# Kernel tuning notes

Hardware: AMD Instinct MI355X
Metric: run time of the kernel (lower is better)

## Reference

```python
import jax, jax.numpy as jnp
import numpy as np

V, D, DC, L, K, H, ND, S, B = 16, 256, 128, 3, 16, 4, 3, 900, 16
HD = D // H
DMETA = 17           # [confidence(1) | layer_id(8) | iter(4) | pass(4)]
DSLOT = DC + DMETA
MAX_ITERS, MAX_PASSES, WRITE_TOK = 2, 2, 64
FLOATS = ['token_embed','segment_embed','slot_embeddings','layer_id_embeddings',
          'Wq_read','Wk_read','Wv_read','Wg_read','bg_read','Wqkv','Wo',
          'Wwk','Wwv','Wwg','bwg','Wout','bout','prev_answer_embed','Wfb','bfb']


def setup_inputs():
    key = jax.random.key(0)
    ks = jax.random.split(key, 24)
    n = lambda i, shape: 0.02 * jax.random.normal(ks[i], shape, dtype=jnp.float32)
    return dict(
        demo_inputs=jax.random.randint(ks[0], (B, ND, S), 0, V),
        demo_outputs=jax.random.randint(ks[1], (B, ND, S), 0, V),
        test_input=jax.random.randint(ks[2], (B, S), 0, V),
        token_embed=n(3, (V, D)), segment_embed=n(4, (2, D)),
        slot_embeddings=n(5, (L, K, DC)), layer_id_embeddings=n(6, (L, 8)),
        Wq_read=n(7, (L, D, DC)), Wk_read=n(8, (L, DSLOT, DC)), Wv_read=n(9, (L, DSLOT, D)),
        Wg_read=n(10, (L, D, 1)), bg_read=jnp.zeros((L, 1)),
        Wqkv=n(11, (L, D, 3 * D)), Wo=n(12, (L, D, D)),
        Wwk=n(13, (L, D, DC)), Wwv=n(14, (L, D, DC)),
        Wwg=n(15, (L, 2 * DC, 1)), bwg=jnp.zeros((L, 1)),
        Wout=n(16, (D, V)), bout=jnp.zeros((V,)),
        prev_answer_embed=n(17, (V, D)),
        Wfb=n(18, (2 * D, D)), bfb=jnp.zeros((D,)),
    )


def make_rope(n, hd):
    inv = 1.0 / (10000.0 ** (jnp.arange(0, hd, 2, dtype=jnp.float32) / hd))
    f = jnp.arange(n, dtype=jnp.float32)[:, None] * inv[None, :]  # [N, hd/2]
    return jnp.cos(f), jnp.sin(f)


def apply_rope(x, cos, sin):  # x: [B,H,N,hd]
    x1, x2 = x[..., ::2], x[..., 1::2]
    r1 = x1 * cos - x2 * sin
    r2 = x1 * sin + x2 * cos
    return jnp.stack([r1, r2], axis=-1).reshape(x.shape)


def layer_step(h, cache, l, it, pas, cos, sin, p):
    Bsz, N, _ = h.shape
    s0 = l * K
    # --- read: cross-attention from sequence to full structured cache ---
    q = h @ p['Wq_read'][l]                                   # [B,N,DC]
    k = cache @ p['Wk_read'][l]                               # [B,LK,DC]
    v = cache @ p['Wv_read'][l]                               # [B,LK,D]
    attn = jax.nn.softmax(jnp.einsum('bnd,bmd->bnm', q, k) / np.float32(np.sqrt(DC)), axis=-1)
    read = jnp.einsum('bnm,bmd->bnd', attn, v)
    rgate = jax.nn.sigmoid(h @ p['Wg_read'][l] + p['bg_read'][l])
    h = h + rgate * read
    # --- linear self-attention with RoPE (use_linear_attention=True) ---
    qh, kh, vh = jnp.split(h @ p['Wqkv'][l], 3, axis=-1)
    heads = lambda x: x.reshape(Bsz, N, H, HD).transpose(0, 2, 1, 3)
    qh, kh, vh = heads(qh), heads(kh), heads(vh)
    qf = jax.nn.elu(apply_rope(qh, cos, sin)) + 1.0
    kf = jax.nn.elu(apply_rope(kh, cos, sin)) + 1.0
    kv = jnp.einsum('bhnd,bhne->bhde', kf, vh)                # [B,H,HD,HD]
    z = 1.0 / (jnp.einsum('bhnd,bhd->bhn', qf, kf.sum(axis=2)) + 1e-6)
    att = jnp.einsum('bhnd,bhde->bhne', qf, kv) * z[..., None]
    h = h + att.transpose(0, 2, 1, 3).reshape(Bsz, N, D) @ p['Wo'][l]
    # --- write: last max_write_tokens tokens -> this layer's slot block ---
    wt = h[:, -WRITE_TOK:]                                    # [B,64,D]
    wk, wv = wt @ p['Wwk'][l], wt @ p['Wwv'][l]               # [B,64,DC]
    sq = cache[:, s0:s0 + K, :DC]                             # slot content queries
    wattn = jax.nn.softmax(jnp.einsum('bkd,bmd->bkm', sq, wk) / np.float32(np.sqrt(DC)), axis=-1)
    new_c = jnp.einsum('bkm,bmd->bkd', wattn, wv)
    wgate = jax.nn.sigmoid(jnp.concatenate([sq, new_c], -1) @ p['Wwg'][l] + p['bwg'][l])
    it_oh = jax.nn.one_hot(min(it, 3), 4, dtype=h.dtype)
    ps_oh = jax.nn.one_hot(min(pas, 3), 4, dtype=h.dtype)
    cache = cache.at[:, s0:s0 + K, :DC].set(sq + wgate * new_c)
    cache = cache.at[:, s0:s0 + K, DC:DC + 1].set(wgate)      # confidence
    cache = cache.at[:, s0:s0 + K, DC + 9:DC + 13].set(jnp.broadcast_to(it_oh, (Bsz, K, 4)))
    cache = cache.at[:, s0:s0 + K, DC + 13:].set(jnp.broadcast_to(ps_oh, (Bsz, K, 4)))
    return h, cache


def _model(p, demo_inputs, demo_outputs, test_input):
    Bsz = test_input.shape[0]
    # interleave demo_in/demo_out pairs then append test input
    demos = jnp.stack([demo_inputs, demo_outputs], axis=2).reshape(Bsz, ND * 2 * S)
    full = jnp.concatenate([demos, test_input], axis=1)       # [B, 6300]
    N = full.shape[1]
    cur = p['token_embed'][full] + p['segment_embed'][0]      # [B,N,D]
    cos, sin = make_rope(N, HD)
    # initial cache: learned content | conf=0 | layer_id | iter=0 | pass=0
    content = jnp.broadcast_to(p['slot_embeddings'].reshape(L * K, DC), (Bsz, L * K, DC))
    lids = jnp.broadcast_to(p['layer_id_embeddings'][:, None, :], (L, K, 8)).reshape(L * K, 8)
    meta = jnp.concatenate([jnp.zeros((L * K, 1)), lids, jnp.zeros((L * K, 8))], axis=-1)
    cache = jnp.concatenate([content, jnp.broadcast_to(meta, (Bsz, L * K, DMETA))], axis=-1)
    ts = ND * 2 * S
    prev_logits = None
    for pas in range(MAX_PASSES):
        if pas > 0:  # answer feedback from previous pass predictions
            pae = p['prev_answer_embed'][jnp.argmax(prev_logits, axis=-1)]
            tr = cur[:, ts:ts + S]
            g = jax.nn.sigmoid(jnp.concatenate([tr, pae], -1) @ p['Wfb'] + p['bfb'])
            cur = cur.at[:, ts:ts + S].set(tr + g * pae)
        h = cur
        for l in range(L):
            for it in range(MAX_ITERS):
                h, cache = layer_step(h, cache, l, it, pas, cos, sin, p)
        prev_logits = h[:, ts:ts + S] @ p['Wout'] + p['bout']  # [B,S,V]
    return prev_logits


def reference(demo_inputs, demo_outputs, test_input, token_embed, segment_embed,
              slot_embeddings, layer_id_embeddings, Wq_read, Wk_read, Wv_read,
              Wg_read, bg_read, Wqkv, Wo, Wwk, Wwv, Wwg, bwg, Wout, bout,
              prev_answer_embed, Wfb, bfb):
    p = dict(zip(FLOATS, (token_embed, segment_embed, slot_embeddings, layer_id_embeddings,
                          Wq_read, Wk_read, Wv_read, Wg_read, bg_read, Wqkv, Wo,
                          Wwk, Wwv, Wwg, bwg, Wout, bout, prev_answer_embed, Wfb, bfb)))
    return _model(p, demo_inputs, demo_outputs, test_input)
```

## Files before the change

kernel.cpp:

```cpp
#include <hip/hip_runtime.h>
#include <math.h>

#define Bz 16
#define Sz 900
#define Vz 16
#define Dz 256
#define DCz 128
#define Hz 4
#define Nz 6300
#define TSz 5400
#define DSLOTz 145
#define NSLOTz 48
#define GXA 99

typedef unsigned short u16;
typedef unsigned int u32;

typedef __bf16 bf16x8 __attribute__((ext_vector_type(8)));
typedef float floatx4 __attribute__((ext_vector_type(4)));
union U8 { bf16x8 v; uint4 q; };

static __device__ __forceinline__ float sigm(float x){ return 1.0f/(1.0f+__expf(-x)); }
static __device__ __forceinline__ void fma4(float4& a, float s, float4 b){ a.x+=s*b.x; a.y+=s*b.y; a.z+=s*b.z; a.w+=s*b.w; }
static __device__ __forceinline__ float dot4(float4 a, float4 b){ return a.x*b.x + a.y*b.y + a.z*b.z + a.w*b.w; }
static __device__ __forceinline__ float4 f4z(){ float4 z; z.x=0.f; z.y=0.f; z.z=0.f; z.w=0.f; return z; }
static __device__ __forceinline__ float elu1(float x){ return x>0.f ? x+1.f : __expf(x); }
static __device__ __forceinline__ float fcomp(float4 v, int i){ return (i==0)?v.x:(i==1)?v.y:(i==2)?v.z:v.w; }

static __device__ __forceinline__ uint hi16(float x){
  uint u = __float_as_uint(x);
  return (u + 0x7fffu + ((u>>16)&1u)) >> 16;
}

typedef const void GV __attribute__((address_space(1)));
typedef void LV __attribute__((address_space(3)));
static __device__ __forceinline__ void gl16(const float* g, float* l){
  __builtin_amdgcn_global_load_lds((GV*)g, (LV*)l, 16, 0, 0);
}
static __device__ __forceinline__ void gl16b(const void* g, void* l){
  __builtin_amdgcn_global_load_lds((GV*)g, (LV*)l, 16, 0, 0);
}

__global__ void k_sentinel(float* out, int nelem){
  int i = blockIdx.x*256 + threadIdx.x;
  if (i < nelem) out[i] = 12345.0f;
}

__global__ void k_zero(float* p, int n){
  int i = blockIdx.x*256 + threadIdx.x;
  if (i < n) p[i] = 0.f;
}

__global__ void k_rope(float* cost, float* sint){
  int i = blockIdx.x*256 + threadIdx.x;
  if (i >= Nz*32) return;
  int n = i>>5, f = i&31;
  double invd = pow(10000.0, -(double)f/32.0);
  double fr = (double)n * invd;
  cost[i] = (float)cos(fr);
  sint[i] = (float)sin(fr);
}

__global__ void k_embed(const int* __restrict__ di, const int* __restrict__ dq,
                        const int* __restrict__ ti, const float* __restrict__ temb,
                        const float* __restrict__ semb, float* __restrict__ h){
  int i = blockIdx.x*256 + threadIdx.x;
  if (i >= Bz*Nz*64) return;
  int dv = i & 63; int bn = i >> 6; int n = bn % Nz; int b = bn / Nz;
  int tok;
  if (n < TSz){
    int nd = n/1800; int r = n - nd*1800;
    tok = (r < Sz) ? di[(b*3+nd)*Sz + r] : dq[(b*3+nd)*Sz + (r-Sz)];
  } else {
    tok = ti[b*Sz + (n-TSz)];
  }
  const float4* e4 = (const float4*)(temb + (size_t)tok*Dz);
  const float4* s4 = (const float4*)semb;
  float4 v = e4[dv]; float4 s = s4[dv];
  v.x += s.x; v.y += s.y; v.z += s.z; v.w += s.w;
  ((float4*)h)[(size_t)bn*64 + dv] = v;
}

__global__ void k_cache_init(const float* __restrict__ slot_emb, const float* __restrict__ lid,
                             float* __restrict__ cache){
  int i = blockIdx.x*256 + threadIdx.x;
  if (i >= Bz*NSLOTz*DSLOTz) return;
  int c = i % DSLOTz; int sc = (i / DSLOTz) % NSLOTz; int l = sc >> 4;
  float v = 0.f;
  if (c < DCz) v = slot_emb[sc*DCz + c];
  else if (c >= 129 && c < 137) v = lid[l*8 + (c-129)];
  cache[i] = v;
}

__global__ void k_pack_w(const float* __restrict__ Wqkv,
                         u16* __restrict__ wh, u16* __restrict__ wl){
  int i = blockIdx.x*256 + threadIdx.x;
  if (i >= 3*65536) return;
  int l = i >> 16; int r = i & 65535;
  int ks = r >> 13; int ct = (r>>9)&15; int lane = (r>>3)&63; int e = r&7;
  int k = ks*32 + ((lane>>4)<<3) + e;
  int c = ct*16 + (lane&15);
  float x = Wqkv[(size_t)l*196608 + (size_t)k*768 + c];
  uint hb = hi16(x);
  uint lb = hi16(x - __uint_as_float(hb<<16));
  wh[i] = (u16)hb; wl[i] = (u16)lb;
}

__global__ void k_pack_wkv(const float* __restrict__ Wqkv,
                           u16* __restrict__ wh, u16* __restrict__ wl){
  int i = blockIdx.x*256 + threadIdx.x;
  if (i >= 3*131072) return;
  int l = i / 131072; int r = i % 131072;
  int ks = r >> 14; int ct = (r>>9)&31; int lane = (r>>3)&63; int e = r&7;
  int k = ks*32 + ((lane>>4)<<3) + e;
  int c = ct*16 + (lane&15);
  float x = Wqkv[(size_t)l*196608 + (size_t)k*768 + 256 + c];
  uint hb = hi16(x);
  uint lb = hi16(x - __uint_as_float(hb<<16));
  wh[i] = (u16)hb; wl[i] = (u16)lb;
}

__global__ void k_pack_wr(const float* __restrict__ Wqr,
                          u16* __restrict__ wh, u16* __restrict__ wl){
  int i = blockIdx.x*256 + threadIdx.x;
  if (i >= 3*32768) return;
  int l = i >> 15; int r = i & 32767;
  int ks = r >> 12; int ct = (r>>9)&7; int lane = (r>>3)&63; int e = r&7;
  int k = ks*32 + ((lane>>4)<<3) + e;
  int c = ct*16 + (lane&15);
  float x = Wqr[(size_t)l*32768 + (size_t)k*DCz + c];
  uint hb = hi16(x);
  uint lb = hi16(x - __uint_as_float(hb<<16));
  wh[i] = (u16)hb; wl[i] = (u16)lb;
}

__global__ void k_pack_p(const float* __restrict__ pmat,
                         u16* __restrict__ ph, u16* __restrict__ pl){
  int i = blockIdx.x*256 + threadIdx.x;
  if (i >= 16*65536) return;
  int b = i >> 16; int r = i & 65535;
  int ks2 = r >> 13; int ct = (r>>9)&15; int lane = (r>>3)&63; int e = r&7;
  int c = ks2*32 + ((lane>>4)<<3) + e;
  int oc = ct*16 + (lane&15);
  float x = pmat[(((size_t)(b*4 + (c>>6)))*64 + (c&63))*256 + oc];
  uint hb = hi16(x);
  uint lb = hi16(x - __uint_as_float(hb<<16));
  ph[i] = (u16)hb; pl[i] = (u16)lb;
}

__global__ __launch_bounds__(384) void k_proj_cache(const float* __restrict__ cache,
    const float* __restrict__ Wk, const float* __restrict__ Wv,
    u16* __restrict__ krh, u16* __restrict__ krl,
    u16* __restrict__ vrh, u16* __restrict__ vrl){
  __shared__ float crow[DSLOTz];
  int b = blockIdx.x / NSLOTz, sc = blockIdx.x % NSLOTz;
  int t = threadIdx.x;
  const float* cp = cache + (size_t)(b*NSLOTz+sc)*DSLOTz;
  if (t < DSLOTz) crow[t] = cp[t];
  __syncthreads();
  if (t < DCz){
    float a = 0.f;
    for (int r2=0;r2<DSLOTz;r2++) a += crow[r2]*Wk[r2*DCz + t];
    uint hb = hi16(a);
    uint lb = hi16(a - __uint_as_float(hb<<16));
    int ks = t>>5, st = sc>>4, lane = (sc&15) | (((t>>3)&3)<<4), e = t&7;
    size_t idx = (size_t)b*6144 + (size_t)(((ks*3+st)*64 + lane)*8 + e);
    krh[idx] = (u16)hb; krl[idx] = (u16)lb;
  } else {
    int d = t - DCz;
    float a = 0.f;
    for (int r2=0;r2<DSLOTz;r2++) a += crow[r2]*Wv[r2*Dz + d];
    uint hb = hi16(a);
    uint lb = hi16(a - __uint_as_float(hb<<16));
    int ot = d>>4, ks2 = sc>>5, lane = (d&15) | (((sc>>3)&3)<<4), e = sc&7;
    size_t idx = (size_t)b*16384 + (size_t)(((ks2*16+ot)*64 + lane)*8 + e);
    vrh[idx] = (u16)hb; vrl[idx] = (u16)lb;
  }
}

#define RA2_BH 0
#define RA2_BL 5120
#define RA2_QBH 10240
#define RA2_QBL 30720
#define RA2_ABH 10240
#define RA2_ABL 20480
#define RA2_G  51200
#define RA2_WG 51456
__global__ __launch_bounds__(256) void k_read_attn(
    float* __restrict__ h,
    const u16* __restrict__ wqh, const u16* __restrict__ wql,
    const u16* __restrict__ krh, const u16* __restrict__ krl,
    const u16* __restrict__ vrh, const u16* __restrict__ vrl,
    const float* __restrict__ Wg, const float* __restrict__ bg,
    float* __restrict__ kvbuf){
  __shared__ float smem[13120];
  char* sb = (char*)smem;
  const int t = threadIdx.x;
  const int b = blockIdx.y;
  const int n0 = blockIdx.x*64;
  const int w = t>>6, lane = t&63, ln = t&15, lq = (t>>4)&3;
  float* hb = h + (size_t)b*Nz*Dz;
  {
    int gid = (b*GXA + blockIdx.x)*256 + t;
    if (gid < Bz*Hz*4160) kvbuf[gid] = 0.f;
  }
  ((float*)(sb+RA2_WG))[t] = Wg[t];
  floatx4 acc[2][4];
  #pragma unroll
  for (int i=0;i<2;i++)
    #pragma unroll
    for (int j=0;j<4;j++){ acc[i][j][0]=0.f; acc[i][j][1]=0.f; acc[i][j][2]=0.f; acc[i][j][3]=0.f; }
  for (int ks=0; ks<8; ks++){
    __syncthreads();
    {
      int n = n0 + (t>>2);
      const float* hp = hb + (size_t)n*Dz + ks*32 + (t&3)*8;
      float x[8];
      if (n < Nz){
        float4 v0 = *(const float4*)(hp);
        float4 v1 = *(const float4*)(hp+4);
        x[0]=v0.x; x[1]=v0.y; x[2]=v0.z; x[3]=v0.w;
        x[4]=v1.x; x[5]=v1.y; x[6]=v1.z; x[7]=v1.w;
      } else {
        #pragma unroll
        for (int e=0;e<8;e++) x[e]=0.f;
      }
      uint hw[4], lw[4];
      #pragma unroll
      for (int e=0;e<4;e++){
        uint h0=hi16(x[2*e]), h1=hi16(x[2*e+1]);
        uint l0=hi16(x[2*e]-__uint_as_float(h0<<16));
        uint l1=hi16(x[2*e+1]-__uint_as_float(h1<<16));
        hw[e]=h0|(h1<<16); lw[e]=l0|(l1<<16);
      }
      int a16 = (((t>>2)*5 + (t&3))<<4);
      *(uint4*)(sb + RA2_BH + a16) = make_uint4(hw[0],hw[1],hw[2],hw[3]);
      *(uint4*)(sb + RA2_BL + a16) = make_uint4(lw[0],lw[1],lw[2],lw[3]);
    }
    __syncthreads();
    U8 bh[4], bl[4];
    #pragma unroll
    for (int nt=0; nt<4; nt++){
      int a16 = (((nt*16+ln)*5 + lq)<<4);
      bh[nt].q = *(const uint4*)(sb + RA2_BH + a16);
      bl[nt].q = *(const uint4*)(sb + RA2_BL + a16);
    }
    #pragma unroll
    for (int mf=0; mf<2; mf++){
      U8 ah, al;
      size_t ai = ((size_t)(ks*8 + w*2 + mf))*512 + lane*8;
      ah.q = *(const uint4*)(wqh + ai);
      al.q = *(const uint4*)(wql + ai);
      #pragma unroll
      for (int nt=0; nt<4; nt++){
        acc[mf][nt] = __builtin_amdgcn_mfma_f32_16x16x32_bf16(ah.v, bh[nt].v, acc[mf][nt], 0,0,0);
        acc[mf][nt] = __builtin_amdgcn_mfma_f32_16x16x32_bf16(ah.v, bl[nt].v, acc[mf][nt], 0,0,0);
        acc[mf][nt] = __builtin_amdgcn_mfma_f32_16x16x32_bf16(al.v, bh[nt].v, acc[mf][nt], 0,0,0);
      }
    }
  }
  {
    int n = t>>2, kq = t&3;
    int nn = n0+n; int nc = (nn < Nz) ? nn : (Nz-1);
    const float* hp = hb + (size_t)nc*Dz + kq*64;
    const float* wgp = (const float*)(sb+RA2_WG) + kq*64;
    float a = 0.f;
    for (int k=0;k<64;k+=4){
      float4 hv = *(const float4*)(hp+k);
      float4 wv = *(const float4*)(wgp+k);
      a += dot4(hv,wv);
    }
    a += __shfl_xor(a,1,64);
    a += __shfl_xor(a,2,64);
    if (kq==0) ((float*)(sb+RA2_G))[n] = a;
  }
  {
    #pragma unroll
    for (int mf=0; mf<2; mf++){
      #pragma unroll
      for (int nt=0; nt<4; nt++){
        float v0 = acc[mf][nt][0], v1 = acc[mf][nt][1];
        float v2 = acc[mf][nt][2], v3 = acc[mf][nt][3];
        uint h0=hi16(v0), h1=hi16(v1), h2=hi16(v2), h3=hi16(v3);
        uint l0=hi16(v0-__uint_as_float(h0<<16));
        uint l1=hi16(v1-__uint_as_float(h1<<16));
        uint l2=hi16(v2-__uint_as_float(h2<<16));
        uint l3=hi16(v3-__uint_as_float(h3<<16));
        int a16 = (((nt*16+ln)*5 + (mf*2 + (lq>>1)))<<4) + ((lq&1)<<3);
        *(uint2*)(sb + RA2_QBH + w*5120 + a16) = make_uint2(h0|(h1<<16), h2|(h3<<16));
        *(uint2*)(sb + RA2_QBL + w*5120 + a16) = make_uint2(l0|(l1<<16), l2|(l3<<16));
      }
    }
  }
  __syncthreads();
  floatx4 sacc[3];
  #pragma unroll
  for (int st=0; st<3; st++){ sacc[st][0]=0.f; sacc[st][1]=0.f; sacc[st][2]=0.f; sacc[st][3]=0.f; }
  for (int ks=0; ks<4; ks++){
    U8 bh, bl;
    int a16 = (((w*16+ln)*5 + lq)<<4);
    bh.q = *(const uint4*)(sb + RA2_QBH + ks*5120 + a16);
    bl.q = *(const uint4*)(sb + RA2_QBL + ks*5120 + a16);
    #pragma unroll
    for (int st=0; st<3; st++){
      U8 ah, al;
      size_t ai = (size_t)b*6144 + ((size_t)(ks*3+st))*512 + lane*8;
      ah.q = *(const uint4*)(krh + ai);
      al.q = *(const uint4*)(krl + ai);
      sacc[st] = __builtin_amdgcn_mfma_f32_16x16x32_bf16(ah.v, bh.v, sacc[st], 0,0,0);
      sacc[st] = __builtin_amdgcn_mfma_f32_16x16x32_bf16(ah.v, bl.v, sacc[st], 0,0,0);
      sacc[st] = __builtin_amdgcn_mfma_f32_16x16x32_bf16(al.v, bh.v, sacc[st], 0,0,0);
    }
  }
  {
    const float scl = 0.088388347648318447f;
    float mx = -1e30f;
    #pragma unroll
    for (int st=0; st<3; st++)
      #pragma unroll
      for (int r=0;r<4;r++){ sacc[st][r] *= scl; mx = fmaxf(mx, sacc[st][r]); }
    mx = fmaxf(mx, __shfl_xor(mx, 16, 64));
    mx = fmaxf(mx, __shfl_xor(mx, 32, 64));
    float su = 0.f;
    #pragma unroll
    for (int st=0; st<3; st++)
      #pragma unroll
      for (int r=0;r<4;r++){ float e = __expf(sacc[st][r]-mx); sacc[st][r]=e; su+=e; }
    su += __shfl_xor(su, 16, 64);
    su += __shfl_xor(su, 32, 64);
    float inv = 1.f/su;
    #pragma unroll
    for (int st=0; st<3; st++)
      #pragma unroll
      for (int r=0;r<4;r++) sacc[st][r] *= inv;
  }
  __syncthreads();
  {
    uint2 ah2[3], al2[3];
    #pragma unroll
    for (int st=0; st<3; st++){
      float v0=sacc[st][0], v1=sacc[st][1], v2=sacc[st][2], v3=sacc[st][3];
      uint h0=hi16(v0), h1=hi16(v1), h2=hi16(v2), h3=hi16(v3);
      uint l0=hi16(v0-__uint_as_float(h0<<16));
      uint l1=hi16(v1-__uint_as_float(h1<<16));
      uint l2=hi16(v2-__uint_as_float(h2<<16));
      uint l3=hi16(v3-__uint_as_float(h3<<16));
      ah2[st] = make_uint2(h0|(h1<<16), h2|(h3<<16));
      al2[st] = make_uint2(l0|(l1<<16), l2|(l3<<16));
    }
    int rb = (w*16+ln)*5;
    int sub = (lq&1)<<3;
    #pragma unroll
    for (int st=0; st<2; st++){
      int a16 = ((rb + st*2 + (lq>>1))<<4) + sub;
      *(uint2*)(sb + RA2_ABH + a16) = ah2[st];
      *(uint2*)(sb + RA2_ABL + a16) = al2[st];
    }
    {
      int a16 = ((rb + (lq>>1))<<4) + sub;
      *(uint2*)(sb + RA2_ABH + 5120 + a16) = ah2[2];
      *(uint2*)(sb + RA2_ABL + 5120 + a16) = al2[2];
      int z16 = ((rb + 2 + (lq>>1))<<4) + sub;
      *(uint2*)(sb + RA2_ABH + 5120 + z16) = make_uint2(0,0);
      *(uint2*)(sb + RA2_ABL + 5120 + z16) = make_uint2(0,0);
    }
  }
  __syncthreads();
  floatx4 o[4][4];
  #pragma unroll
  for (int i=0;i<4;i++)
    #pragma unroll
    for (int j=0;j<4;j++){ o[i][j][0]=0.f; o[i][j][1]=0.f; o[i][j][2]=0.f; o[i][j][3]=0.f; }
  #pragma unroll
  for (int ks2=0; ks2<2; ks2++){
    U8 bh[4], bl[4];
    #pragma unroll
    for (int nt=0; nt<4; nt++){
      int a16 = (((nt*16+ln)*5 + lq)<<4);
      bh[nt].q = *(const uint4*)(sb + RA2_ABH + ks2*5120 + a16);
      bl[nt].q = *(const uint4*)(sb + RA2_ABL + ks2*5120 + a16);
    }
    #pragma unroll
    for (int mf=0; mf<4; mf++){
      U8 ah, al;
      size_t ai = (size_t)b*16384 + ((size_t)(ks2*16 + w*4 + mf))*512 + lane*8;
      ah.q = *(const uint4*)(vrh + ai);
      al.q = *(const uint4*)(vrl + ai);
      #pragma unroll
      for (int nt=0; nt<4; nt++){
        o[mf][nt] = __builtin_amdgcn_mfma_f32_16x16x32_bf16(ah.v, bh[nt].v, o[mf][nt], 0,0,0);
        o[mf][nt] = __builtin_amdgcn_mfma_f32_16x16x32_bf16(ah.v, bl[nt].v, o[mf][nt], 0,0,0);
        o[mf][nt] = __builtin_amdgcn_mfma_f32_16x16x32_bf16(al.v, bh[nt].v, o[mf][nt], 0,0,0);
      }
    }
  }
  float bg0 = bg[0];
  #pragma unroll
  for (int nt=0; nt<4; nt++){
    int n = n0 + nt*16 + ln;
    if (n < Nz){
      float gv = sigm(((const float*)(sb+RA2_G))[nt*16+ln] + bg0);
      #pragma unroll
      for (int mf=0; mf<4; mf++){
        float* hp = hb + (size_t)n*Dz + w*64 + mf*16 + lq*4;
        float4 hv = *(const float4*)hp;
        hv.x += gv*o[mf][nt][0];
        hv.y += gv*o[mf][nt][1];
        hv.z += gv*o[mf][nt][2];
        hv.w += gv*o[mf][nt][3];
        *(float4*)hp = hv;
      }
    }
  }
}

__global__ __launch_bounds__(256) void k_kv(
    const float* __restrict__ h,
    const u16* __restrict__ wh, const u16* __restrict__ wl,
    const float* __restrict__ cost, const float* __restrict__ sint,
    float* __restrict__ kvbuf){
  __shared__ float smem[8704];
  char* sb = (char*)smem;
  const int t = threadIdx.x;
  const int b = blockIdx.y;
  const int n0 = blockIdx.x*64;
  const int w = t>>6;
  const int lane = t&63;
  const int ln = t&15;
  const int lq = (t>>4)&3;
  const float* hb = h + (size_t)b*Nz*Dz;
  floatx4 acc[2][4][4];
  #pragma unroll
  for (int cp=0;cp<2;cp++)
    #pragma unroll
    for (int i=0;i<4;i++)
      #pragma unroll
      for (int j=0;j<4;j++){ acc[cp][i][j][0]=0.f; acc[cp][i][j][1]=0.f; acc[cp][i][j][2]=0.f; acc[cp][i][j][3]=0.f; }

  const int hrow = t>>2, hcol = t&3;
  const float* hbase = hb + (size_t)(n0+hrow)*Dz + hcol*8;
  const int hvalid = (n0+hrow) < Nz;
  const int a16w = ((hrow*5 + hcol)<<4);

  auto load_h = [&](int ks, float x[8]){
    if (hvalid){
      float4 v0 = *(const float4*)(hbase + ks*32);
      float4 v1 = *(const float4*)(hbase + ks*32 + 4);
      x[0]=v0.x; x[1]=v0.y; x[2]=v0.z; x[3]=v0.w;
      x[4]=v1.x; x[5]=v1.y; x[6]=v1.z; x[7]=v1.w;
    } else {
      #pragma unroll
      for (int e=0;e<8;e++) x[e]=0.f;
    }
  };
  auto cvt_write = [&](const float x[8], int buf){
    uint hw[4], lw[4];
    #pragma unroll
    for (int e=0;e<4;e++){
      uint h0=hi16(x[2*e]), h1=hi16(x[2*e+1]);
      uint l0=hi16(x[2*e]-__uint_as_float(h0<<16));
      uint l1=hi16(x[2*e+1]-__uint_as_float(h1<<16));
      hw[e]=h0|(h1<<16); lw[e]=l0|(l1<<16);
    }
    *(uint4*)(sb + buf*10240 + a16w) = make_uint4(hw[0],hw[1],hw[2],hw[3]);
    *(uint4*)(sb + buf*10240 + 5120 + a16w) = make_uint4(lw[0],lw[1],lw[2],lw[3]);
  };

  { float x0[8]; load_h(0, x0); cvt_write(x0, 0); }
  for (int ks=0; ks<8; ks++){
    __syncthreads();
    float xn[8];
    if (ks < 7) load_h(ks+1, xn);
    const int cb = ks&1;
    U8 bh[4], bl[4];
    #pragma unroll
    for (int nt=0; nt<4; nt++){
      int a16 = (((nt*16+ln)*5 + lq)<<4);
      bh[nt].q = *(const uint4*)(sb + cb*10240 + a16);
      bl[nt].q = *(const uint4*)(sb + cb*10240 + 5120 + a16);
    }
    #pragma unroll
    for (int cp=0; cp<2; cp++){
      #pragma unroll
      for (int mf=0; mf<4; mf++){
        U8 ah, al;
        size_t ai = ((size_t)(ks*32 + cp*16 + w*4 + mf))*512 + lane*8;
        ah.q = *(const uint4*)(wh + ai);
        al.q = *(const uint4*)(wl + ai);
        #pragma unroll
        for (int nt=0; nt<4; nt++){
          acc[cp][mf][nt] = __builtin_amdgcn_mfma_f32_16x16x32_bf16(ah.v, bh[nt].v, acc[cp][mf][nt], 0,0,0);
          acc[cp][mf][nt] = __builtin_amdgcn_mfma_f32_16x16x32_bf16(ah.v, bl[nt].v, acc[cp][mf][nt], 0,0,0);
          acc[cp][mf][nt] = __builtin_amdgcn_mfma_f32_16x16x32_bf16(al.v, bh[nt].v, acc[cp][mf][nt], 0,0,0);
        }
      }
    }
    if (ks < 7) cvt_write(xn, cb^1);
  }
  #pragma unroll
  for (int mf=0; mf<4; mf++){
    #pragma unroll
    for (int nt=0; nt<4; nt++){
      int n = n0 + nt*16 + ln;
      int valid = (n < Nz);
      int nc = valid ? n : (Nz-1);
      int pi = mf*8 + lq*2;
      float2 c2 = *(const float2*)(cost + (size_t)nc*32 + pi);
      float2 s2 = *(const float2*)(sint + (size_t)nc*32 + pi);
      float q0 = acc[0][mf][nt][0], q1 = acc[0][mf][nt][1];
      float q2 = acc[0][mf][nt][2], q3 = acc[0][mf][nt][3];
      float r0 = elu1(q0*c2.x - q1*s2.x);
      float r1 = elu1(q0*s2.x + q1*c2.x);
      float r2 = elu1(q2*c2.y - q3*s2.y);
      float r3 = elu1(q2*s2.y + q3*c2.y);
      acc[0][mf][nt][0] = valid ? r0 : 0.f;
      acc[0][mf][nt][1] = valid ? r1 : 0.f;
      acc[0][mf][nt][2] = valid ? r2 : 0.f;
      acc[0][mf][nt][3] = valid ? r3 : 0.f;
    }
  }
  const int d = t&63, q4 = t>>6;
  float* kfL = smem;
  float* vL  = smem + 4352;
  for (int g=0; g<4; g++){
    __syncthreads();
    if (w == g){
      #pragma unroll
      for (int mf=0; mf<4; mf++){
        #pragma unroll
        for (int nt=0; nt<4; nt++){
          int n = nt*16 + ln;
          int cc = mf*16 + lq*4;
          *(float4*)(kfL + n*68 + cc) = make_float4(acc[0][mf][nt][0],acc[0][mf][nt][1],acc[0][mf][nt][2],acc[0][mf][nt][3]);
          *(float4*)(vL  + n*68 + cc) = make_float4(acc[1][mf][nt][0],acc[1][mf][nt][1],acc[1][mf][nt][2],acc[1][mf][nt][3]);
        }
      }
    }
    __syncthreads();
    float4 kvacc[4];
    #pragma unroll
    for (int u=0;u<4;u++) kvacc[u]=f4z();
    float ksl = 0.f;
    for (int row=0; row<64; row++){
      float kd = kfL[row*68 + d];
      ksl += kd;
      const float4* vp = (const float4*)(vL + row*68);
      #pragma unroll
      for (int u=0;u<4;u++) fma4(kvacc[u], kd, vp[q4*4+u]);
    }
    float* kq = kvbuf + ((size_t)(b*Hz + g))*4160;
    #pragma unroll
    for (int u=0;u<4;u++){
      int e = q4*16 + 4*u;
      atomicAdd(&kq[(e+0)*64+d], kvacc[u].x);
      atomicAdd(&kq[(e+1)*64+d], kvacc[u].y);
      atomicAdd(&kq[(e+2)*64+d], kvacc[u].z);
      atomicAdd(&kq[(e+3)*64+d], kvacc[u].w);
    }
    if (q4==0) atomicAdd(&kq[4096+d], ksl);
  }
}

__global__ __launch_bounds__(256) void k_pmat(const float* __restrict__ kvbuf,
    const float* __restrict__ Wo, float* __restrict__ pmat){
  __shared__ float smem[8448];
  const int t = threadIdx.x;
  const int bh = blockIdx.x;
  const int hh = bh & 3;
  const int c0 = t&15, rr = t>>4;
  const float* kvp = kvbuf + (size_t)bh*4160;
  for (int id=t; id<4096; id+=256){
    int e=id>>6, d=id&63;
    smem[e*68+d] = kvp[id];
  }
  float4 acc[4][4];
  #pragma unroll
  for (int i=0;i<4;i++){
    #pragma unroll
    for (int j=0;j<4;j++) acc[i][j]=f4z();
  }
  for (int kt=0; kt<64; kt+=16){
    __syncthreads();
    for (int id=t; id<1024; id+=256){
      int wr=id>>6, cf=id&63;
      ((float4*)(smem+4352))[wr*64+cf] = ((const float4*)(Wo + (size_t)(hh*64+kt+wr)*256))[cf];
    }
    __syncthreads();
    for (int kk=0; kk<16; kk++){
      float4 a4 = *(const float4*)(smem + (kt+kk)*68 + 4*rr);
      const float4* wrow = (const float4*)(smem+4352) + kk*64;
      float4 w0=wrow[c0], w1=wrow[c0+16], w2=wrow[c0+32], w3=wrow[c0+48];
      #pragma unroll
      for (int i=0;i<4;i++){
        float ac = fcomp(a4,i);
        fma4(acc[i][0],ac,w0); fma4(acc[i][1],ac,w1); fma4(acc[i][2],ac,w2); fma4(acc[i][3],ac,w3);
      }
    }
  }
  float* Pp = pmat + (size_t)bh*16384;
  #pragma unroll
  for (int i=0;i<4;i++){
    #pragma unroll
    for (int j=0;j<4;j++) ((float4*)Pp)[(4*rr+i)*64 + c0 + 16*j] = acc[i][j];
  }
}

#define KA_KS 20480
__global__ __launch_bounds__(256) void k_att(
    float* __restrict__ h,
    const u16* __restrict__ wqh, const u16* __restrict__ wql,
    const u16* __restrict__ pth, const u16* __restrict__ ptl,
    const float* __restrict__ kvbuf,
    const float* __restrict__ cost, const float* __restrict__ sint){
  __shared__ float smem[5376];
  char* sb = (char*)smem;
  const int t = threadIdx.x;
  const int b = blockIdx.y;
  const int n0 = blockIdx.x*64;
  const int w = t>>6;
  const int lane = t&63;
  const int ln = t&15;
  const int lq = (t>>4)&3;
  float* hb = h + (size_t)b*Nz*Dz;
  ((float*)(sb+KA_KS))[t] = kvbuf[(size_t)(b*Hz + w)*4160 + 4096 + lane];

  const int hrow = t>>2, hcol = t&3;
  const float* hbase = hb + (size_t)(n0+hrow)*Dz + hcol*8;
  const int hvalid = (n0+hrow) < Nz;
  const int a16w = ((hrow*5 + hcol)<<4);
  auto load_h = [&](int ks, float x[8]){
    if (hvalid){
      float4 v0 = *(const float4*)(hbase + ks*32);
      float4 v1 = *(const float4*)(hbase + ks*32 + 4);
      x[0]=v0.x; x[1]=v0.y; x[2]=v0.z; x[3]=v0.w;
      x[4]=v1.x; x[5]=v1.y; x[6]=v1.z; x[7]=v1.w;
    } else {
      #pragma unroll
      for (int e=0;e<8;e++) x[e]=0.f;
    }
  };
  auto cvt_write = [&](const float x[8], int buf){
    uint hw[4], lw[4];
    #pragma unroll
    for (int e=0;e<4;e++){
      uint h0=hi16(x[2*e]), h1=hi16(x[2*e+1]);
      uint l0=hi16(x[2*e]-__uint_as_float(h0<<16));
      uint l1=hi16(x[2*e+1]-__uint_as_float(h1<<16));
      hw[e]=h0|(h1<<16); lw[e]=l0|(l1<<16);
    }
    *(uint4*)(sb + buf*10240 + a16w) = make_uint4(hw[0],hw[1],hw[2],hw[3]);
    *(uint4*)(sb + buf*10240 + 5120 + a16w) = make_uint4(lw[0],lw[1],lw[2],lw[3]);
  };

  floatx4 acc[4][4];
  #pragma unroll
  for (int i=0;i<4;i++)
    #pragma unroll
    for (int j=0;j<4;j++){ acc[i][j][0]=0.f; acc[i][j][1]=0.f; acc[i][j][2]=0.f; acc[i][j][3]=0.f; }

  { float x0[8]; load_h(0, x0); cvt_write(x0, 0); }
  for (int ks=0; ks<8; ks++){
    __syncthreads();
    float xn[8];
    if (ks < 7) load_h(ks+1, xn);
    const int cb = ks&1;
    U8 bh[4], bl[4];
    #pragma unroll
    for (int nt=0; nt<4; nt++){
      int a16 = (((nt*16+ln)*5 + lq)<<4);
      bh[nt].q = *(const uint4*)(sb + cb*10240 + a16);
      bl[nt].q = *(const uint4*)(sb + cb*10240 + 5120 + a16);
    }
    #pragma unroll
    for (int mf=0; mf<4; mf++){
      U8 ah, al;
      size_t ai = ((size_t)(ks*16 + w*4 + mf))*512 + lane*8;
      ah.q = *(const uint4*)(wqh + ai);
      al.q = *(const uint4*)(wql + ai);
      #pragma unroll
      for (int nt=0; nt<4; nt++){
        acc[mf][nt] = __builtin_amdgcn_mfma_f32_16x16x32_bf16(ah.v, bh[nt].v, acc[mf][nt], 0,0,0);
        acc[mf][nt] = __builtin_amdgcn_mfma_f32_16x16x32_bf16(ah.v, bl[nt].v, acc[mf][nt], 0,0,0);
        acc[mf][nt] = __builtin_amdgcn_mfma_f32_16x16x32_bf16(al.v, bh[nt].v, acc[mf][nt], 0,0,0);
      }
    }
    if (ks < 7) cvt_write(xn, cb^1);
  }
  uint2 qzh[4][4], qzl[4][4];
  {
    float4 ks4[4];
    #pragma unroll
    for (int mf=0; mf<4; mf++)
      ks4[mf] = *(const float4*)(sb + KA_KS + ((w*64 + mf*16 + lq*4)<<2));
    float psum[4] = {0.f,0.f,0.f,0.f};
    #pragma unroll
    for (int mf=0; mf<4; mf++){
      #pragma unroll
      for (int nt=0; nt<4; nt++){
        int n = n0 + nt*16 + ln;
        int nc = (n < Nz) ? n : (Nz-1);
        int pi = mf*8 + lq*2;
        float2 c2 = *(const float2*)(cost + (size_t)nc*32 + pi);
        float2 s2 = *(const float2*)(sint + (size_t)nc*32 + pi);
        float q0 = acc[mf][nt][0], q1 = acc[mf][nt][1];
        float q2 = acc[mf][nt][2], q3 = acc[mf][nt][3];
        float r0 = elu1(q0*c2.x - q1*s2.x);
        float r1 = elu1(q0*s2.x + q1*c2.x);
        float r2 = elu1(q2*c2.y - q3*s2.y);
        float r3 = elu1(q2*s2.y + q3*c2.y);
        acc[mf][nt][0]=r0; acc[mf][nt][1]=r1; acc[mf][nt][2]=r2; acc[mf][nt][3]=r3;
        psum[nt] += r0*ks4[mf].x + r1*ks4[mf].y + r2*ks4[mf].z + r3*ks4[mf].w;
      }
    }
    float zt[4];
    #pragma unroll
    for (int nt=0; nt<4; nt++){
      float p = psum[nt];
      p += __shfl_xor(p, 16, 64);
      p += __shfl_xor(p, 32, 64);
      zt[nt] = 1.f/(p + 1e-6f);
    }
    #pragma unroll
    for (int mf=0; mf<4; mf++){
      #pragma unroll
      for (int nt=0; nt<4; nt++){
        float v0 = acc[mf][nt][0]*zt[nt];
        float v1 = acc[mf][nt][1]*zt[nt];
        float v2 = acc[mf][nt][2]*zt[nt];
        float v3 = acc[mf][nt][3]*zt[nt];
        uint h0=hi16(v0), h1=hi16(v1), h2=hi16(v2), h3=hi16(v3);
        qzh[mf][nt] = make_uint2(h0|(h1<<16), h2|(h3<<16));
        uint l0=hi16(v0-__uint_as_float(h0<<16));
        uint l1=hi16(v1-__uint_as_float(h1<<16));
        uint l2=hi16(v2-__uint_as_float(h2<<16));
        uint l3=hi16(v3-__uint_as_float(h3<<16));
        qzl[mf][nt] = make_uint2(l0|(l1<<16), l2|(l3<<16));
      }
    }
  }
  auto write_slice = [&](int s, int buf){
    #pragma unroll
    for (int mm=0; mm<2; mm++){
      int mf = ((s&1)<<1) + mm;
      int g = (mm<<1) + (lq>>1);
      int sub = (lq&1)*8;
      #pragma unroll
      for (int nt=0; nt<4; nt++){
        int a16 = (((nt*16+ln)*5 + g)<<4) + sub;
        *(uint2*)(sb + buf*10240 + a16) = qzh[mf][nt];
        *(uint2*)(sb + buf*10240 + 5120 + a16) = qzl[mf][nt];
      }
    }
  };
  floatx4 acc2[4][4];
  #pragma unroll
  for (int i=0;i<4;i++)
    #pragma unroll
    for (int j=0;j<4;j++){ acc2[i][j][0]=0.f; acc2[i][j][1]=0.f; acc2[i][j][2]=0.f; acc2[i][j][3]=0.f; }
  __syncthreads();
  if (w == 0) write_slice(0, 0);
  for (int ks2=0; ks2<8; ks2++){
    __syncthreads();
    if (ks2 < 7 && w == ((ks2+1)>>1)) write_slice(ks2+1, (ks2+1)&1);
    const int cb = ks2&1;
    U8 bh[4], bl[4];
    #pragma unroll
    for (int nt=0; nt<4; nt++){
      int a16 = (((nt*16+ln)*5 + lq)<<4);
      bh[nt].q = *(const uint4*)(sb + cb*10240 + a16);
      bl[nt].q = *(const uint4*)(sb + cb*10240 + 5120 + a16);
    }
    #pragma unroll
    for (int mf=0; mf<4; mf++){
      U8 ah, al;
      size_t ai = ((size_t)((b*8 + ks2)*16 + w*4 + mf))*512 + lane*8;
      ah.q = *(const uint4*)(pth + ai);
      al.q = *(const uint4*)(ptl + ai);
      #pragma unroll
      for (int nt=0; nt<4; nt++){
        acc2[mf][nt] = __builtin_amdgcn_mfma_f32_16x16x32_bf16(ah.v, bh[nt].v, acc2[mf][nt], 0,0,0);
        acc2[mf][nt] = __builtin_amdgcn_mfma_f32_16x16x32_bf16(ah.v, bl[nt].v, acc2[mf][nt], 0,0,0);
        acc2[mf][nt] = __builtin_amdgcn_mfma_f32_16x16x32_bf16(al.v, bh[nt].v, acc2[mf][nt], 0,0,0);
      }
    }
  }
  #pragma unroll
  for (int mf=0; mf<4; mf++){
    #pragma unroll
    for (int nt=0; nt<4; nt++){
      int n = n0 + nt*16 + ln;
      if (n < Nz){
        float* hp = hb + (size_t)n*Dz + w*64 + mf*16 + lq*4;
        float4 hv = *(const float4*)hp;
        hv.x += acc2[mf][nt][0];
        hv.y += acc2[mf][nt][1];
        hv.z += acc2[mf][nt][2];
        hv.w += acc2[mf][nt][3];
        *(float4*)hp = hv;
      }
    }
  }
}

__global__ __launch_bounds__(256) void k_wkv(const float* __restrict__ h,
    const float* __restrict__ Wwk, const float* __restrict__ Wwv,
    float* __restrict__ wkbuf, float* __restrict__ wvbuf){
  __shared__ float wtL[16*257];
  int t = threadIdx.x;
  int b = blockIdx.y, m0 = blockIdx.x*16;
  const float* hb = h + ((size_t)b*Nz + (Nz-64))*Dz;
  for (int i=t;i<16*Dz;i+=256){ int r=i>>8,c=i&255; wtL[r*257+c] = hb[(size_t)(m0+r)*Dz + c]; }
  __syncthreads();
  int r=t>>4, c0=t&15;
  float4 ak0=f4z(),ak1=f4z(),av0=f4z(),av1=f4z();
  for (int kk=0;kk<Dz;kk++){
    float hv = wtL[r*257+kk];
    const float4* wk4 = (const float4*)(Wwk + (size_t)kk*DCz);
    const float4* wv4 = (const float4*)(Wwv + (size_t)kk*DCz);
    fma4(ak0,hv,wk4[c0]); fma4(ak1,hv,wk4[c0+16]);
    fma4(av0,hv,wv4[c0]); fma4(av1,hv,wv4[c0+16]);
  }
  float4* ok = (float4*)(wkbuf + (size_t)(b*64 + m0+r)*DCz);
  float4* ov = (float4*)(wvbuf + (size_t)(b*64 + m0+r)*DCz);
  ok[c0]=ak0; ok[c0+16]=ak1; ov[c0]=av0; ov[c0+16]=av1;
}

__global__ __launch_bounds__(256) void k_cache_upd(float* __restrict__ cache,
    const float* __restrict__ wkbuf, const float* __restrict__ wvbuf,
    const float* __restrict__ Wwg, const float* __restrict__ bwg,
    int s0, int it, int pas){
  __shared__ float sqL[16*132];
  __shared__ float wkL[64*132];
  __shared__ float wat[16*68];
  __shared__ float ncL[16*132];
  __shared__ float wg[16];
  int t = threadIdx.x; int b = blockIdx.x;
  for (int i=t;i<16*DCz;i+=256){ int k2=i>>7,c=i&127; sqL[k2*132+c] = cache[((size_t)(b*NSLOTz)+s0+k2)*DSLOTz + c]; }
  for (int i=t;i<64*DCz;i+=256){ int m=i>>7,c=i&127; wkL[m*132+c] = wkbuf[(size_t)(b*64+m)*DCz+c]; }
  __syncthreads();
  {
    int k2 = t>>4;
    const float4* s4 = (const float4*)(sqL) + k2*33;
    for (int mm=0;mm<4;mm++){
      int m = (t&15) + 16*mm;
      const float4* k4 = (const float4*)(wkL) + m*33;
      float a=0.f;
      for (int d4=0;d4<32;d4++) a += dot4(s4[d4], k4[d4]);
      wat[k2*68+m] = a * 0.088388347648318447f;
    }
  }
  __syncthreads();
  if (t<16){
    float mx=-1e30f;
    for (int m=0;m<64;m++) mx = fmaxf(mx, wat[t*68+m]);
    float su=0.f;
    for (int m=0;m<64;m++){ float e=__expf(wat[t*68+m]-mx); wat[t*68+m]=e; su+=e; }
    float inv=1.f/su;
    for (int m=0;m<64;m++) wat[t*68+m]*=inv;
  }
  __syncthreads();
  {
    int k2=t>>4, c0=t&15;
    float4 a0=f4z(), a1=f4z();
    const float4* wvg = (const float4*)(wvbuf + (size_t)b*64*DCz);
    for (int m=0;m<64;m++){
      float a = wat[k2*68+m];
      fma4(a0,a,wvg[m*32+c0]); fma4(a1,a,wvg[m*32+c0+16]);
    }
    ((float4*)ncL)[k2*33+c0]=a0; ((float4*)ncL)[k2*33+16+c0]=a1;
  }
  __syncthreads();
  if (t<16){
    float a = bwg[0];
    for (int d2=0; d2<DCz; d2++) a += sqL[t*132+d2]*Wwg[d2] + ncL[t*132+d2]*Wwg[DCz+d2];
    wg[t] = sigm(a);
  }
  __syncthreads();
  for (int i=t;i<16*DCz;i+=256){
    int k2=i>>7,c=i&127;
    cache[((size_t)(b*NSLOTz)+s0+k2)*DSLOTz + c] = sqL[k2*132+c] + wg[k2]*ncL[k2*132+c];
  }
  if (t<16){
    float* cp = cache + ((size_t)(b*NSLOTz)+s0+t)*DSLOTz;
    cp[128] = wg[t];
    cp[137] = (it==0)?1.f:0.f; cp[138] = (it==1)?1.f:0.f; cp[139]=0.f; cp[140]=0.f;
    cp[141] = (pas==0)?1.f:0.f; cp[142] = (pas==1)?1.f:0.f; cp[143]=0.f; cp[144]=0.f;
  }
}

__global__ __launch_bounds__(256) void k_logits(const float* __restrict__ h,
    const float* __restrict__ Wout, const float* __restrict__ bout, float* __restrict__ out){
  __shared__ float hl[16*257];
  int t = threadIdx.x; int row0 = blockIdx.x*16;
  for (int i=t;i<16*Dz;i+=256){
    int rr=i>>8,c=i&255; int row=row0+rr; int b=row/Sz, s=row-b*Sz;
    hl[rr*257+c] = h[((size_t)b*Nz + TSz + s)*Dz + c];
  }
  __syncthreads();
  int rr = t>>4, v = t&15;
  float a = bout[v];
  for (int c=0;c<Dz;c++) a += hl[rr*257+c]*Wout[c*Vz + v];
  out[(size_t)(row0+rr)*Vz + v] = a;
}

__global__ __launch_bounds__(256) void k_feedback(float* __restrict__ h,
    const float* __restrict__ logits0, const float* __restrict__ pae,
    const float* __restrict__ Wfb, const float* __restrict__ bfb){
  __shared__ float trL[16*257];
  __shared__ float paeL[16*257];
  __shared__ int amL[16];
  int t = threadIdx.x; int b = blockIdx.y; int s0 = blockIdx.x*16;
  if (t<16){
    int s = s0+t; int am=0;
    if (s < Sz){
      const float* lg = logits0 + (size_t)(b*Sz+s)*Vz;
      float best = lg[0];
      for (int v=1;v<16;v++){ if (lg[v] > best){ best=lg[v]; am=v; } }
    }
    amL[t]=am;
  }
  for (int i=t;i<16*Dz;i+=256){
    int rr=i>>8,c=i&255; int s=s0+rr;
    trL[rr*257+c] = (s<Sz)? h[((size_t)b*Nz + TSz + s)*Dz + c] : 0.f;
  }
  __syncthreads();
  for (int i=t;i<16*Dz;i+=256){ int rr=i>>8,c=i&255; paeL[rr*257+c] = pae[(size_t)amL[rr]*Dz + c]; }
  __syncthreads();
  int r=t>>4, c0=t&15;
  float4 acc[4]; acc[0]=f4z(); acc[1]=f4z(); acc[2]=f4z(); acc[3]=f4z();
  for (int kk=0;kk<Dz;kk++){
    float xv = trL[r*257+kk];
    const float4* wr = (const float4*)(Wfb + (size_t)kk*Dz);
    fma4(acc[0],xv,wr[c0]); fma4(acc[1],xv,wr[c0+16]); fma4(acc[2],xv,wr[c0+32]); fma4(acc[3],xv,wr[c0+48]);
  }
  for (int kk=0;kk<Dz;kk++){
    float xv = paeL[r*257+kk];
    const float4* wr = (const float4*)(Wfb + (size_t)(Dz+kk)*Dz);
    fma4(acc[0],xv,wr[c0]); fma4(acc[1],xv,wr[c0+16]); fma4(acc[2],xv,wr[c0+32]); fma4(acc[3],xv,wr[c0+48]);
  }
  int s = s0+r;
  if (s < Sz){
    float* cp = h + ((size_t)b*Nz + TSz + s)*Dz;
    #pragma unroll
    for (int j=0;j<4;j++){
      float vals[4] = {acc[j].x, acc[j].y, acc[j].z, acc[j].w};
      #pragma unroll
      for (int q2=0;q2<4;q2++){
        int c = (c0+16*j)*4 + q2;
        float g = sigm(vals[q2] + bfb[c]);
        cp[c] = trL[r*257+c] + g*paeL[r*257+c];
      }
    }
  }
}

extern "C" void kernel_launch(void* const* d_in, const int* in_sizes, int n_in,
                              void* d_out, int out_size, void* d_ws, size_t ws_size,
                              hipStream_t stream){
  (void)in_sizes; (void)n_in;
  const int*   demo_in   = (const int*)d_in[0];
  const int*   demo_out  = (const int*)d_in[1];
  const int*   test_in   = (const int*)d_in[2];
  const float* token_emb = (const float*)d_in[3];
  const float* seg_emb   = (const float*)d_in[4];
  const float* slot_emb  = (const float*)d_in[5];
  const float* lid_emb   = (const float*)d_in[6];
  const float* Wq_read   = (const float*)d_in[7];
  const float* Wk_read   = (const float*)d_in[8];
  const float* Wv_read   = (const float*)d_in[9];
  const float* Wg_read   = (const float*)d_in[10];
  const float* bg_read   = (const float*)d_in[11];
  const float* Wqkv      = (const float*)d_in[12];
  const float* Wo        = (const float*)d_in[13];
  const float* Wwk       = (const float*)d_in[14];
  const float* Wwv       = (const float*)d_in[15];
  const float* Wwg       = (const float*)d_in[16];
  const float* bwg       = (const float*)d_in[17];
  const float* Wout      = (const float*)d_in[18];
  const float* bout      = (const float*)d_in[19];
  const float* pae       = (const float*)d_in[20];
  const float* Wfb       = (const float*)d_in[21];
  const float* bfb       = (const float*)d_in[22];

  char* wsb = (char*)d_ws;
  size_t off = 0;
  auto alloc = [&](size_t bytes)->char*{
    char* p = wsb + off;
    off += (bytes + 255) & ~(size_t)255;
    return p;
  };
  float* hbuf   = (float*)alloc((size_t)Bz*Nz*Dz*4);
  float* cache  = (float*)alloc((size_t)Bz*NSLOTz*DSLOTz*4);
  float* kvbuf  = (float*)alloc((size_t)Bz*Hz*4160*4);
  float* pmat   = (float*)alloc((size_t)Bz*Hz*64*256*4);
  float* wkbuf  = (float*)alloc((size_t)Bz*64*DCz*4);
  float* wvbuf  = (float*)alloc((size_t)Bz*64*DCz*4);
  float* logits0= (float*)alloc((size_t)Bz*Sz*Vz*4);
  float* cost   = (float*)alloc((size_t)Nz*32*4);
  float* sint   = (float*)alloc((size_t)Nz*32*4);
  u16*   wqth   = (u16*)alloc((size_t)3*65536*2);
  u16*   wqtl   = (u16*)alloc((size_t)3*65536*2);
  u16*   pth    = (u16*)alloc((size_t)16*65536*2);
  u16*   ptl    = (u16*)alloc((size_t)16*65536*2);
  u16*   wkvh   = (u16*)alloc((size_t)3*131072*2);
  u16*   wkvl   = (u16*)alloc((size_t)3*131072*2);
  u16*   wqrh   = (u16*)alloc((size_t)3*32768*2);
  u16*   wqrl   = (u16*)alloc((size_t)3*32768*2);
  u16*   krh    = (u16*)alloc((size_t)Bz*6144*2);
  u16*   krl    = (u16*)alloc((size_t)Bz*6144*2);
  u16*   vrh    = (u16*)alloc((size_t)Bz*16384*2);
  u16*   vrl    = (u16*)alloc((size_t)Bz*16384*2);

  if (off > ws_size){
    k_sentinel<<<(out_size+255)/256, 256, 0, stream>>>((float*)d_out, out_size);
    return;
  }

  k_rope<<<(Nz*32+255)/256, 256, 0, stream>>>(cost, sint);
  k_cache_init<<<(Bz*NSLOTz*DSLOTz+255)/256, 256, 0, stream>>>(slot_emb, lid_emb, cache);
  k_pack_w<<<768, 256, 0, stream>>>(Wqkv, wqth, wqtl);
  k_pack_wkv<<<1536, 256, 0, stream>>>(Wqkv, wkvh, wkvl);
  k_pack_wr<<<384, 256, 0, stream>>>(Wq_read, wqrh, wqrl);
  k_zero<<<512, 256, 0, stream>>>((float*)vrh, Bz*16384/2);
  k_zero<<<512, 256, 0, stream>>>((float*)vrl, Bz*16384/2);

  for (int pas=0; pas<2; pas++){
    k_embed<<<(Bz*Nz*64+255)/256, 256, 0, stream>>>(demo_in, demo_out, test_in, token_emb, seg_emb, hbuf);
    if (pas==1)
      k_feedback<<<dim3(57,Bz), 256, 0, stream>>>(hbuf, logits0, pae, Wfb, bfb);
    for (int l=0; l<3; l++){
      for (int it=0; it<2; it++){
        k_proj_cache<<<Bz*NSLOTz, 384, 0, stream>>>(cache,
            Wk_read + (size_t)l*DSLOTz*DCz, Wv_read + (size_t)l*DSLOTz*Dz,
            krh, krl, vrh, vrl);
        k_read_attn<<<dim3(GXA,Bz), 256, 0, stream>>>(hbuf,
            wqrh + (size_t)l*32768, wqrl + (size_t)l*32768,
            krh, krl, vrh, vrl,
            Wg_read + (size_t)l*Dz, bg_read + l, kvbuf);
        k_kv<<<dim3(GXA,Bz), 256, 0, stream>>>(hbuf,
            wkvh + (size_t)l*131072, wkvl + (size_t)l*131072, cost, sint, kvbuf);
        k_pmat<<<Bz*Hz, 256, 0, stream>>>(kvbuf, Wo + (size_t)l*Dz*Dz, pmat);
        k_pack_p<<<4096, 256, 0, stream>>>(pmat, pth, ptl);
        k_att<<<dim3(GXA,Bz), 256, 0, stream>>>(hbuf,
            wqth + (size_t)l*65536, wqtl + (size_t)l*65536, pth, ptl,
            kvbuf, cost, sint);
        k_wkv<<<dim3(4,Bz), 256, 0, stream>>>(hbuf,
            Wwk + (size_t)l*Dz*DCz, Wwv + (size_t)l*Dz*DCz, wkbuf, wvbuf);
        k_cache_upd<<<Bz, 256, 0, stream>>>(cache, wkbuf, wvbuf,
            Wwg + (size_t)l*2*DCz, bwg + l, l*16, it, pas);
      }
    }
    float* outp = (pas==0) ? logits0 : (float*)d_out;
    k_logits<<<900, 256, 0, stream>>>(hbuf, Wout, bout, outp);
  }
}
```

Before: 7.902 ms.

## Double-buffer read-attention LDS tiles and shrink shared memory footprint

In the read-attention kernel, the h-tile split-bf16 staging is now double-buffered: the next k-slice is loaded from global memory while the MFMAs on the current slice run, which removes one barrier per step. The Q slices are kept in registers and each wave writes its slice into a rotating two-buffer LDS region instead of all four slices at once. Shared memory drops from about 52KB to about 22KB, so more blocks can be resident per CU. In exchange there are extra registers for the prefetched data and the Q fragments, and a barrier per step in the score loop.

```diff
diff --git a/kernel.cpp b/kernel.cpp
--- a/kernel.cpp
+++ b/kernel.cpp
@@ -178,14 +178,8 @@
   }
 }
 
-#define RA2_BH 0
-#define RA2_BL 5120
-#define RA2_QBH 10240
-#define RA2_QBL 30720
-#define RA2_ABH 10240
-#define RA2_ABL 20480
-#define RA2_G  51200
-#define RA2_WG 51456
+#define RB_G  20480
+#define RB_WG 20736
 __global__ __launch_bounds__(256) void k_read_attn(
     float* __restrict__ h,
     const u16* __restrict__ wqh, const u16* __restrict__ wql,
@@ -193,7 +187,7 @@
     const u16* __restrict__ vrh, const u16* __restrict__ vrl,
     const float* __restrict__ Wg, const float* __restrict__ bg,
     float* __restrict__ kvbuf){
-  __shared__ float smem[13120];
+  __shared__ float smem[5440];
   char* sb = (char*)smem;
   const int t = threadIdx.x;
   const int b = blockIdx.y;
@@ -204,46 +198,53 @@
     int gid = (b*GXA + blockIdx.x)*256 + t;
     if (gid < Bz*Hz*4160) kvbuf[gid] = 0.f;
   }
-  ((float*)(sb+RA2_WG))[t] = Wg[t];
+  ((float*)(sb+RB_WG))[t] = Wg[t];
+
+  const int hrow = t>>2, hcol = t&3;
+  const float* hbase = hb + (size_t)(n0+hrow)*Dz + hcol*8;
+  const int hvalid = (n0+hrow) < Nz;
+  const int a16w = ((hrow*5 + hcol)<<4);
+  auto load_h = [&](int ks, float x[8]){
+    if (hvalid){
+      float4 v0 = *(const float4*)(hbase + ks*32);
+      float4 v1 = *(const float4*)(hbase + ks*32 + 4);
+      x[0]=v0.x; x[1]=v0.y; x[2]=v0.z; x[3]=v0.w;
+      x[4]=v1.x; x[5]=v1.y; x[6]=v1.z; x[7]=v1.w;
+    } else {
+      #pragma unroll
+      for (int e=0;e<8;e++) x[e]=0.f;
+    }
+  };
+  auto cvt_write = [&](const float x[8], int buf){
+    uint hw[4], lw[4];
+    #pragma unroll
+    for (int e=0;e<4;e++){
+      uint h0=hi16(x[2*e]), h1=hi16(x[2*e+1]);
+      uint l0=hi16(x[2*e]-__uint_as_float(h0<<16));
+      uint l1=hi16(x[2*e+1]-__uint_as_float(h1<<16));
+      hw[e]=h0|(h1<<16); lw[e]=l0|(l1<<16);
+    }
+    *(uint4*)(sb + buf*10240 + a16w) = make_uint4(hw[0],hw[1],hw[2],hw[3]);
+    *(uint4*)(sb + buf*10240 + 5120 + a16w) = make_uint4(lw[0],lw[1],lw[2],lw[3]);
+  };
+
   floatx4 acc[2][4];
   #pragma unroll
   for (int i=0;i<2;i++)
     #pragma unroll
     for (int j=0;j<4;j++){ acc[i][j][0]=0.f; acc[i][j][1]=0.f; acc[i][j][2]=0.f; acc[i][j][3]=0.f; }
+  { float x0[8]; load_h(0, x0); cvt_write(x0, 0); }
   for (int ks=0; ks<8; ks++){
     __syncthreads();
-    {
-      int n = n0 + (t>>2);
-      const float* hp = hb + (size_t)n*Dz + ks*32 + (t&3)*8;
-      float x[8];
-      if (n < Nz){
-        float4 v0 = *(const float4*)(hp);
-        float4 v1 = *(const float4*)(hp+4);
-        x[0]=v0.x; x[1]=v0.y; x[2]=v0.z; x[3]=v0.w;
-        x[4]=v1.x; x[5]=v1.y; x[6]=v1.z; x[7]=v1.w;
-      } else {
-        #pragma unroll
-        for (int e=0;e<8;e++) x[e]=0.f;
-      }
-      uint hw[4], lw[4];
-      #pragma unroll
-      for (int e=0;e<4;e++){
-        uint h0=hi16(x[2*e]), h1=hi16(x[2*e+1]);
-        uint l0=hi16(x[2*e]-__uint_as_float(h0<<16));
-        uint l1=hi16(x[2*e+1]-__uint_as_float(h1<<16));
-        hw[e]=h0|(h1<<16); lw[e]=l0|(l1<<16);
-      }
-      int a16 = (((t>>2)*5 + (t&3))<<4);
-      *(uint4*)(sb + RA2_BH + a16) = make_uint4(hw[0],hw[1],hw[2],hw[3]);
-      *(uint4*)(sb + RA2_BL + a16) = make_uint4(lw[0],lw[1],lw[2],lw[3]);
-    }
-    __syncthreads();
+    float xn[8];
+    if (ks < 7) load_h(ks+1, xn);
+    const int cb = ks&1;
     U8 bh[4], bl[4];
     #pragma unroll
     for (int nt=0; nt<4; nt++){
       int a16 = (((nt*16+ln)*5 + lq)<<4);
-      bh[nt].q = *(const uint4*)(sb + RA2_BH + a16);
-      bl[nt].q = *(const uint4*)(sb + RA2_BL + a16);
+      bh[nt].q = *(const uint4*)(sb + cb*10240 + a16);
+      bl[nt].q = *(const uint4*)(sb + cb*10240 + 5120 + a16);
     }
     #pragma unroll
     for (int mf=0; mf<2; mf++){
@@ -258,12 +259,13 @@
         acc[mf][nt] = __builtin_amdgcn_mfma_f32_16x16x32_bf16(al.v, bh[nt].v, acc[mf][nt], 0,0,0);
       }
     }
+    if (ks < 7) cvt_write(xn, cb^1);
   }
   {
     int n = t>>2, kq = t&3;
     int nn = n0+n; int nc = (nn < Nz) ? nn : (Nz-1);
     const float* hp = hb + (size_t)nc*Dz + kq*64;
-    const float* wgp = (const float*)(sb+RA2_WG) + kq*64;
+    const float* wgp = (const float*)(sb+RB_WG) + kq*64;
     float a = 0.f;
     for (int k=0;k<64;k+=4){
       float4 hv = *(const float4*)(hp+k);
@@ -272,35 +274,50 @@
     }
     a += __shfl_xor(a,1,64);
     a += __shfl_xor(a,2,64);
-    if (kq==0) ((float*)(sb+RA2_G))[n] = a;
-  }
-  {
+    if (kq==0) ((float*)(sb+RB_G))[n] = a;
+  }
+  uint2 qh[2][4], ql[2][4];
+  #pragma unroll
+  for (int mf=0; mf<2; mf++){
+    #pragma unroll
+    for (int nt=0; nt<4; nt++){
+      float v0 = acc[mf][nt][0], v1 = acc[mf][nt][1];
+      float v2 = acc[mf][nt][2], v3 = acc[mf][nt][3];
+      uint h0=hi16(v0), h1=hi16(v1), h2=hi16(v2), h3=hi16(v3);
+      uint l0=hi16(v0-__uint_as_float(h0<<16));
+      uint l1=hi16(v1-__uint_as_float(h1<<16));
+      uint l2=hi16(v2-__uint_as_float(h2<<16));
+      uint l3=hi16(v3-__uint_as_float(h3<<16));
+      qh[mf][nt] = make_uint2(h0|(h1<<16), h2|(h3<<16));
+      ql[mf][nt] = make_uint2(l0|(l1<<16), l2|(l3<<16));
+    }
+  }
+  auto write_qslice = [&](int buf){
     #pragma unroll
     for (int mf=0; mf<2; mf++){
+      int g = mf*2 + (lq>>1);
+      int sub = (lq&1)<<3;
       #pragma unroll
       for (int nt=0; nt<4; nt++){
-        float v0 = acc[mf][nt][0], v1 = acc[mf][nt][1];
-        float v2 = acc[mf][nt][2], v3 = acc[mf][nt][3];
-        uint h0=hi16(v0), h1=hi16(v1), h2=hi16(v2), h3=hi16(v3);
-        uint l0=hi16(v0-__uint_as_float(h0<<16));
-        uint l1=hi16(v1-__uint_as_float(h1<<16));
-        uint l2=hi16(v2-__uint_as_float(h2<<16));
-        uint l3=hi16(v3-__uint_as_float(h3<<16));
-        int a16 = (((nt*16+ln)*5 + (mf*2 + (lq>>1)))<<4) + ((lq&1)<<3);
-        *(uint2*)(sb + RA2_QBH + w*5120 + a16) = make_uint2(h0|(h1<<16), h2|(h3<<16));
-        *(uint2*)(sb + RA2_QBL + w*5120 + a16) = make_uint2(l0|(l1<<16), l2|(l3<<16));
-      }
-    }
-  }
-  __syncthreads();
+        int a16 = (((nt*16+ln)*5 + g)<<4) + sub;
+        *(uint2*)(sb + buf*10240 + a16) = qh[mf][nt];
+        *(uint2*)(sb + buf*10240 + 5120 + a16) = ql[mf][nt];
+      }
+    }
+  };
   floatx4 sacc[3];
   #pragma unroll
   for (int st=0; st<3; st++){ sacc[st][0]=0.f; sacc[st][1]=0.f; sacc[st][2]=0.f; sacc[st][3]=0.f; }
+  __syncthreads();
+  if (w == 0) write_qslice(0);
   for (int ks=0; ks<4; ks++){
+    __syncthreads();
+    if (ks < 3 && w == ks+1) write_qslice((ks+1)&1);
+    const int cb = ks&1;
     U8 bh, bl;
     int a16 = (((w*16+ln)*5 + lq)<<4);
-    bh.q = *(const uint4*)(sb + RA2_QBH + ks*5120 + a16);
-    bl.q = *(const uint4*)(sb + RA2_QBL + ks*5120 + a16);
+    bh.q = *(const uint4*)(sb + cb*10240 + a16);
+    bl.q = *(const uint4*)(sb + cb*10240 + 5120 + a16);
     #pragma unroll
     for (int st=0; st<3; st++){
       U8 ah, al;
@@ -353,16 +370,16 @@
     #pragma unroll
     for (int st=0; st<2; st++){
       int a16 = ((rb + st*2 + (lq>>1))<<4) + sub;
-      *(uint2*)(sb + RA2_ABH + a16) = ah2[st];
-      *(uint2*)(sb + RA2_ABL + a16) = al2[st];
+      *(uint2*)(sb + a16) = ah2[st];
+      *(uint2*)(sb + 5120 + a16) = al2[st];
     }
     {
       int a16 = ((rb + (lq>>1))<<4) + sub;
-      *(uint2*)(sb + RA2_ABH + 5120 + a16) = ah2[2];
-      *(uint2*)(sb + RA2_ABL + 5120 + a16) = al2[2];
+      *(uint2*)(sb + 10240 + a16) = ah2[2];
+      *(uint2*)(sb + 10240 + 5120 + a16) = al2[2];
       int z16 = ((rb + 2 + (lq>>1))<<4) + sub;
-      *(uint2*)(sb + RA2_ABH + 5120 + z16) = make_uint2(0,0);
-      *(uint2*)(sb + RA2_ABL + 5120 + z16) = make_uint2(0,0);
+      *(uint2*)(sb + 10240 + z16) = make_uint2(0,0);
+      *(uint2*)(sb + 10240 + 5120 + z16) = make_uint2(0,0);
     }
   }
   __syncthreads();
@@ -377,8 +394,8 @@
     #pragma unroll
     for (int nt=0; nt<4; nt++){
       int a16 = (((nt*16+ln)*5 + lq)<<4);
-      bh[nt].q = *(const uint4*)(sb + RA2_ABH + ks2*5120 + a16);
-      bl[nt].q = *(const uint4*)(sb + RA2_ABL + ks2*5120 + a16);
+      bh[nt].q = *(const uint4*)(sb + ks2*10240 + a16);
+      bl[nt].q = *(const uint4*)(sb + ks2*10240 + 5120 + a16);
     }
     #pragma unroll
     for (int mf=0; mf<4; mf++){
@@ -399,7 +416,7 @@
   for (int nt=0; nt<4; nt++){
     int n = n0 + nt*16 + ln;
     if (n < Nz){
-      float gv = sigm(((const float*)(sb+RA2_G))[nt*16+ln] + bg0);
+      float gv = sigm(((const float*)(sb+RB_G))[nt*16+ln] + bg0);
       #pragma unroll
       for (int mf=0; mf<4; mf++){
         float* hp = hb + (size_t)n*Dz + w*64 + mf*16 + lq*4;
```

New measurement: 7.754 ms. About the same (-1.9%).
